# Optimization experiments

Hardware: AMD Instinct MI355X
Metric: run time of the kernel (lower is better)

## Reference

```python
import jax, jax.numpy as jnp
import numpy as np

K = 7
SIZE = (129, 129)


def _conv2d(x, w, b, pad):
    # x: NCHW, w: OIHW
    y = jax.lax.conv_general_dilated(
        x, w, window_strides=(1, 1), padding=[(pad, pad), (pad, pad)],
        dimension_numbers=("NCHW", "OIHW", "NCHW"))
    return y + b[None, :, None, None]


def _upsample_bilinear(x, size):
    # matches torch nn.Upsample(mode='bilinear', align_corners=False)
    b, c = x.shape[0], x.shape[1]
    return jax.image.resize(x, (b, c, size[0], size[1]), method="bilinear")


def _spatially_variant_conv(kernels, features, k):
    # kernels: [b,k,k,h,w], features: [b,c,h,w]
    # equivalent to unfold + einsum('bcklhw,bklhw->bchw') but without the
    # huge im2col intermediate: accumulate over the k*k shifted views.
    b, c, h, w = features.shape
    p = k // 2
    fp = jnp.pad(features, ((0, 0), (0, 0), (p, p), (p, p)))
    out = jnp.zeros_like(features)
    for i in range(k):
        for j in range(k):
            out = out + fp[:, :, i:i + h, j:j + w] * kernels[:, i, j][:, None]
    return out


def setup_inputs() -> dict:
    key = jax.random.key(0)
    ks = jax.random.split(key, 9)
    s = 0.05
    return {
        "current_frame_low_features": jax.random.normal(ks[0], (2, 128, 33, 33), jnp.float32),
        "key_frame_low_features": jax.random.normal(ks[1], (2, 128, 33, 33), jnp.float32),
        "key_frame_high_features": jax.random.normal(ks[2], (2, 256, 129, 129), jnp.float32),
        "w_reduce": jax.random.normal(ks[3], (256, 128, 3, 3), jnp.float32) * s,
        "b_reduce": jnp.zeros((256,), jnp.float32),
        "w_conv2": jax.random.normal(ks[4], (256, 512, 3, 3), jnp.float32) * s,
        "b_conv2": jnp.zeros((256,), jnp.float32),
        "w_conv3": jax.random.normal(ks[5], (K * K, 256, 1, 1), jnp.float32) * s,
        "b_conv3": jnp.zeros((K * K,), jnp.float32),
    }


def reference(current_frame_low_features, key_frame_low_features,
              key_frame_high_features, w_reduce, b_reduce,
              w_conv2, b_conv2, w_conv3, b_conv3):
    cur_up = _upsample_bilinear(current_frame_low_features, SIZE)
    key_up = _upsample_bilinear(key_frame_low_features, SIZE)

    # KernelWeightPredictor (shared conv_reduce weights for both frames)
    cur = jax.nn.relu(_conv2d(cur_up, w_reduce, b_reduce, 1))
    key = jax.nn.relu(_conv2d(key_up, w_reduce, b_reduce, 1))
    x = jax.nn.relu(_conv2d(jnp.concatenate((cur, key), axis=1), w_conv2, b_conv2, 1))
    x = jax.nn.relu(_conv2d(x, w_conv3, b_conv3, 0))
    x = jax.nn.softmax(x, axis=1)  # [b, k*k, H, W]
    b = x.shape[0]
    kernels = x.reshape(b, K, K, SIZE[0], SIZE[1])

    return _spatially_variant_conv(kernels, key_frame_high_features, K)
```

## Files before the change

kernel.cpp:

```cpp
#include <hip/hip_runtime.h>

typedef unsigned short u16;
typedef unsigned int   u32;
typedef __attribute__((ext_vector_type(8))) short s16x8;
typedef __attribute__((ext_vector_type(4))) float f32x4;
typedef __attribute__((ext_vector_type(4), aligned(4))) float f32x4u;
typedef __attribute__((ext_vector_type(4))) u32   u32x4;
typedef __attribute__((ext_vector_type(4))) u16   u16x4;

#define NPIX 16641
#define HP   131
#define FPH  135
#define FPW  136
#define FPC  18360


__device__ __forceinline__ u16 f2bf(float f) {
    u32 b = __builtin_bit_cast(u32, f);
    return (u16)((b + 0x7fffu + ((b >> 16) & 1u)) >> 16);
}
__device__ __forceinline__ float bf2f(u16 u) {
    return __builtin_bit_cast(float, ((u32)u) << 16);
}

__device__ __forceinline__ void async_cp16(const void* g, void* l) {
    __builtin_amdgcn_global_load_lds(
        (const __attribute__((address_space(1))) u32*)g,
        (__attribute__((address_space(3))) u32*)l, 16, 0, 0);
}

__global__ __launch_bounds__(256) void zero_border(u16* __restrict__ U,
                                                   u16* __restrict__ S1) {
    const int plane = blockIdx.y;
    const bool isU = plane < 4;
    const int C = isU ? 128 : 512;
    const int cpp = C / 8;
    int e = blockIdx.x * 256 + threadIdx.x;
    if (e >= 520 * cpp) return;
    int pix = e / cpp, ch = e - pix * cpp;
    int r, c;
    if (pix < 131)      { r = 0;   c = pix; }
    else if (pix < 262) { r = 130; c = pix - 131; }
    else { int j = pix - 262; r = 1 + (j >> 1); c = (j & 1) ? 130 : 0; }
    int img = isU ? plane : (plane - 4);
    u16* base = (isU ? U : S1) + ((long)(img * HP + r) * HP + c) * C + ch * 8;
    u32x4 z = {0u, 0u, 0u, 0u};
    *(u32x4*)base = z;
}

__global__ __launch_bounds__(256) void prep_weights(
        const float* __restrict__ wr, const float* __restrict__ w2,
        const float* __restrict__ w3,
        u16* __restrict__ Wt1, u16* __restrict__ Wt2, float* __restrict__ w3t) {
    int i = blockIdx.x * 256 + threadIdx.x;
    if (i < 294912) {
        int tap = i / 32768, r = i & 32767;
        int co = r >> 7, ci = r & 127;
        Wt1[i] = f2bf(wr[(co * 128 + ci) * 9 + tap]);
    } else if (i < 1474560) {
        int j = i - 294912;
        int tap = j / 131072, r = j & 131071;
        int co = r >> 9, ci = r & 511;
        Wt2[j] = f2bf(w2[(co * 512 + ci) * 9 + tap]);
    } else if (i < 1487104) {
        int j = i - 1474560;
        int c = j / 49, t = j - c * 49;
        w3t[j] = w3[t * 256 + c];
    }
}

__global__ __launch_bounds__(256) void upsample(
        const float* __restrict__ cur, const float* __restrict__ key,
        u16* __restrict__ U) {
    __shared__ float rows[2][128][33];
    const int y = blockIdx.x;
    const int img = blockIdx.y;
    const int frame = img >> 1, bb = img & 1;
    const float* src = (frame ? key : cur) + (long)bb * 128 * 1089;
    const float scale = 33.0f / 129.0f;
    float syf = (y + 0.5f) * scale - 0.5f;
    int sy0 = (int)floorf(syf);
    float wy = syf - (float)sy0;
    int sy0c = sy0 < 0 ? 0 : sy0;
    int sy1c = (sy0 + 1 > 32) ? 32 : sy0 + 1;
    for (int e = threadIdx.x; e < 2 * 128 * 33; e += 256) {
        int rr = e / 4224;
        int rem = e - rr * 4224;
        int c = rem / 33, sx = rem - c * 33;
        rows[rr][c][sx] = src[((long)c * 33 + (rr ? sy1c : sy0c)) * 33 + sx];
    }
    __syncthreads();
    u16* dst = U + ((long)(img * HP + (y + 1)) * HP + 1) * 128;
    for (int e = threadIdx.x; e < 129 * 128; e += 256) {
        int x = e >> 7, c = e & 127;
        float sxf = (x + 0.5f) * scale - 0.5f;
        int sx0 = (int)floorf(sxf);
        float wx = sxf - (float)sx0;
        int sx0c = sx0 < 0 ? 0 : sx0;
        int sx1c = (sx0 + 1 > 32) ? 32 : sx0 + 1;
        float v0 = rows[0][c][sx0c] * (1.f - wx) + rows[0][c][sx1c] * wx;
        float v1 = rows[1][c][sx0c] * (1.f - wx) + rows[1][c][sx1c] * wx;
        dst[(long)x * 128 + c] = f2bf(v0 * (1.f - wy) + v1 * wy);
    }
}

template<int CIN, int MODE, int NWORK, int SPLIT>
__global__ __launch_bounds__(256) void conv_mfma(
        const u16* __restrict__ In, const u16* __restrict__ Wt,
        const float* __restrict__ bias,
        u16* __restrict__ Out0, u16* __restrict__ Out1) {
    constexpr int KC  = CIN / 32;
    constexpr int NS  = 9 * KC;
    constexpr int NSH = NS / SPLIT;
    constexpr int PER = (NWORK + 7) / 8;
    __shared__ u16 As[3][128 * 32];
    __shared__ u16 Bs[3][128 * 32];

    const int id = blockIdx.x;
    const int work = (id & 7) * PER + (id >> 3);
    if (work >= NWORK) return;
    int w = work;
    const int m0 = (w & 1) * 128; w >>= 1;
    int half = 0;
    if (SPLIT == 2) { half = w & 1; w >>= 1; }
    const int xi  = w % 131;
    const int img = w / 131;
    const int p0  = xi * 128;

    const int t    = threadIdx.x;
    const int srow = t >> 2;
    const int scol = ((((t & 3) - (srow >> 1)) & 3) * 8);
    long ub[2];
    #pragma unroll
    for (int is = 0; is < 2; ++is) {
        int p = p0 + srow + is * 64; if (p > NPIX - 1) p = NPIX - 1;
        int y = p / 129, x = p - y * 129;
        ub[is] = ((long)(img * HP + y) * HP + x) * CIN + scol;
    }
    const long wb0 = (long)(m0 + srow) * CIN + scol;

    const int lane = t & 63;
    const int wave = t >> 6;
    const int wm = wave & 1, wn = wave >> 1;
    const int lm = lane & 15, lq = lane >> 4;
    const int koff = (((lq + (lm >> 1)) & 3) * 8);

    auto stage = [&](int s, int buf) {
        const int tap = s / KC;
        const int kc  = (s - tap * KC) * 32;
        const int ky = tap / 3, kx = tap - ky * 3;
        const long toff = (long)(ky * HP + kx) * CIN + kc;
        const u16* WtT = Wt + (long)tap * 256 * CIN + kc;
        char* Aw = (char*)&As[buf][0] + wave * 1024;
        char* Bw = (char*)&Bs[buf][0] + wave * 1024;
        async_cp16(WtT + wb0,             Aw);
        async_cp16(WtT + wb0 + 64L * CIN, Aw + 4096);
        async_cp16(In + ub[0] + toff,     Bw);
        async_cp16(In + ub[1] + toff,     Bw + 4096);
    };

    f32x4 acc[4][4];
    f32x4 zero = {0.f, 0.f, 0.f, 0.f};
    #pragma unroll
    for (int mt = 0; mt < 4; ++mt)
        #pragma unroll
        for (int nt = 0; nt < 4; ++nt) acc[mt][nt] = zero;

    const int s0 = half * NSH;
    stage(s0 + 0, 0);
    stage(s0 + 1, 1);
    #pragma unroll 2
    for (int i = 0; i < NSH; ++i) {
        const int buf = i % 3;
        if (i < NSH - 1) asm volatile("s_waitcnt vmcnt(4)" ::: "memory");
        else             asm volatile("s_waitcnt vmcnt(0)" ::: "memory");
        __builtin_amdgcn_s_barrier();
        asm volatile("" ::: "memory");
        if (i + 2 < NSH) stage(s0 + i + 2, (i + 2) % 3);
        s16x8 fa[4], fb[4];
        #pragma unroll
        for (int mt = 0; mt < 4; ++mt)
            fa[mt] = *(const s16x8*)&As[buf][(wm * 64 + mt * 16 + lm) * 32 + koff];
        #pragma unroll
        for (int nt = 0; nt < 4; ++nt)
            fb[nt] = *(const s16x8*)&Bs[buf][(wn * 64 + nt * 16 + lm) * 32 + koff];
        #pragma unroll
        for (int mt = 0; mt < 4; ++mt)
            #pragma unroll
            for (int nt = 0; nt < 4; ++nt)
                acc[mt][nt] = __builtin_amdgcn_mfma_f32_16x16x32_bf16(
                    fa[mt], fb[nt], acc[mt][nt], 0, 0, 0);
    }

    u16* OutBf = half ? Out1 : Out0;
    #pragma unroll
    for (int nt = 0; nt < 4; ++nt) {
        int p = p0 + wn * 64 + nt * 16 + lm;
        if (p > NPIX - 1) continue;
        long obase;
        if (MODE == 0) {
            int y = p / 129, x = p - y * 129;
            int bb = img & 1, frame = img >> 1;
            obase = ((long)(bb * HP + (y + 1)) * HP + (x + 1)) * 512 + frame * 256;
        } else {
            obase = ((long)img * NPIX + p) * 256;
        }
        #pragma unroll
        for (int mt = 0; mt < 4; ++mt) {
            int co = m0 + wm * 64 + mt * 16 + lq * 4;
            f32x4 bv = *(const f32x4*)(bias + co);
            if (MODE == 0) {
                float v0 = fmaxf(acc[mt][nt][0] + bv[0], 0.f);
                float v1 = fmaxf(acc[mt][nt][1] + bv[1], 0.f);
                float v2 = fmaxf(acc[mt][nt][2] + bv[2], 0.f);
                float v3 = fmaxf(acc[mt][nt][3] + bv[3], 0.f);
                u16x4 o = { f2bf(v0), f2bf(v1), f2bf(v2), f2bf(v3) };
                *(u16x4*)(OutBf + obase + co) = o;
            } else {
                float bs = half ? 0.f : 1.f;
                u16x4 o = { f2bf(acc[mt][nt][0] + bs * bv[0]),
                            f2bf(acc[mt][nt][1] + bs * bv[1]),
                            f2bf(acc[mt][nt][2] + bs * bv[2]),
                            f2bf(acc[mt][nt][3] + bs * bv[3]) };
                *(u16x4*)(OutBf + obase + co) = o;
            }
        }
    }
}

__global__ __launch_bounds__(256) void fpad(
        const float* __restrict__ F, float* __restrict__ Fp) {
    int id = blockIdx.x * 256 + threadIdx.x;
    if (id >= 2 * 256 * FPH * (FPW / 4)) return;
    int ck = id % (FPW / 4);
    int r  = id / (FPW / 4);
    int yy = r % FPH;
    int ch = r / FPH;
    int y = yy - 3;
    f32x4 v;
    const float* Fr = F + ((long)ch * 129 + y) * 129;
    #pragma unroll
    for (int j = 0; j < 4; ++j) {
        int x = ck * 4 + j - 3;
        bool in = ((unsigned)x < 129u) && ((unsigned)y < 129u);
        v[j] = in ? Fr[x] : 0.f;
    }
    *(f32x4*)(Fp + (long)ch * FPC + yy * FPW + ck * 4) = v;
}

__global__ __launch_bounds__(256) void conv3_softmax(
        const u16* __restrict__ Xa, const u16* __restrict__ Xb,
        const float* __restrict__ W3t, const float* __restrict__ b3,
        float* __restrict__ P) {
    __shared__ float red[3][64][50];
    const int t = threadIdx.x;
    const int pl = t & 63, sub = t >> 6;
    const int idx = blockIdx.x * 64 + pl;
    const bool valid = idx < 2 * NPIX;
    float l[49];
    #pragma unroll
    for (int k = 0; k < 49; ++k) l[k] = 0.f;
    if (valid) {
        const s16x8* xra = (const s16x8*)(Xa + (long)idx * 256 + sub * 64);
        const s16x8* xrb = (const s16x8*)(Xb + (long)idx * 256 + sub * 64);
        #pragma unroll 1
        for (int cb = 0; cb < 8; ++cb) {
            s16x8 av = xra[cb];
            s16x8 bv = xrb[cb];
            #pragma unroll
            for (int j = 0; j < 8; ++j) {
                float xc = fmaxf(bf2f((u16)av[j]) + bf2f((u16)bv[j]), 0.f);
                const float* wrow = W3t + (sub * 64 + cb * 8 + j) * 49;
                #pragma unroll
                for (int k = 0; k < 49; ++k) l[k] = fmaf(wrow[k], xc, l[k]);
            }
        }
    }
    if (sub) {
        #pragma unroll
        for (int k = 0; k < 49; ++k) red[sub - 1][pl][k] = l[k];
    }
    __syncthreads();
    if (!sub && valid) {
        float m = 0.f;
        #pragma unroll
        for (int k = 0; k < 49; ++k) {
            l[k] = fmaxf(l[k] + red[0][pl][k] + red[1][pl][k] + red[2][pl][k]
                         + b3[k], 0.f);
            m = fmaxf(m, l[k]);
        }
        float ssum = 0.f;
        #pragma unroll
        for (int k = 0; k < 49; ++k) { l[k] = __expf(l[k] - m); ssum += l[k]; }
        float inv = 1.f / ssum;
        int bb = idx / NPIX, pix = idx - bb * NPIX;
        float* Pp = P + ((long)bb * NPIX + pix) * 52;
        #pragma unroll
        for (int k = 0; k < 49; ++k) Pp[k] = l[k] * inv;
    }
}

__global__ __launch_bounds__(256) void svconv(
        const float* __restrict__ Fp, const float* __restrict__ P,
        float* __restrict__ Out) {
    const int id = blockIdx.x;
    const int work = (id & 7) * 1056 + (id >> 3);
    const int cg   = work & 63;
    const int tile = work >> 6;
    const int img  = tile / 66, ti = tile % 66;
    const int pix  = ti * 256 + threadIdx.x;
    if (pix >= NPIX) return;
    const int y = pix / 129, x = pix - y * 129;

    float w[52];
    const f32x4* Pp = (const f32x4*)(P + ((long)img * NPIX + pix) * 52);
    #pragma unroll
    for (int k = 0; k < 13; ++k) *(f32x4*)&w[k * 4] = Pp[k];

    const float* Fc0 = Fp + (long)(img * 256 + cg * 4) * FPC + (long)y * FPW + x;
    float acc[4];
    #pragma unroll
    for (int c4 = 0; c4 < 4; ++c4) {
        const float* Fc = Fc0 + c4 * FPC;
        float a = 0.f;
        #pragma unroll
        for (int ky = 0; ky < 7; ++ky) {
            const float* rp = Fc + ky * FPW;
            f32x4u v0 = *(const f32x4u*)rp;
            f32x4u v1 = *(const f32x4u*)(rp + 4);
            const float* wr = &w[ky * 7];
            a = fmaf(wr[0], v0[0], a);
            a = fmaf(wr[1], v0[1], a);
            a = fmaf(wr[2], v0[2], a);
            a = fmaf(wr[3], v0[3], a);
            a = fmaf(wr[4], v1[0], a);
            a = fmaf(wr[5], v1[1], a);
            a = fmaf(wr[6], v1[2], a);
        }
        acc[c4] = a;
    }
    float* Ob = Out + ((long)(img * 256 + cg * 4)) * NPIX + pix;
    Ob[0] = acc[0];
    Ob[(long)NPIX] = acc[1];
    Ob[2L * NPIX] = acc[2];
    Ob[3L * NPIX] = acc[3];
}

extern "C" void kernel_launch(void* const* d_in, const int* in_sizes, int n_in,
                              void* d_out, int out_size, void* d_ws, size_t ws_size,
                              hipStream_t stream) {
    const float* cur      = (const float*)d_in[0];
    const float* key      = (const float*)d_in[1];
    const float* Fhigh    = (const float*)d_in[2];
    const float* w_reduce = (const float*)d_in[3];
    const float* b_reduce = (const float*)d_in[4];
    const float* w_conv2  = (const float*)d_in[5];
    const float* b_conv2  = (const float*)d_in[6];
    const float* w_conv3  = (const float*)d_in[7];
    const float* b_conv3  = (const float*)d_in[8];

    if (ws_size < 89798656UL) return;

    char* ws = (char*)d_ws;
    u16*   U     = (u16*)(ws + 0);
    u16*   S1    = (u16*)(ws + 17572864);
    float* Fpad  = (float*)(ws + 0);
    float* P     = (float*)(ws + 37601280);
    u16*   Wt1   = (u16*)(ws + 52718592);
    u16*   Wt2   = (u16*)(ws + 53308416);
    u16*   out2a = (u16*)(ws + 55667712);
    u16*   out2b = (u16*)(ws + 72708096);
    float* w3t   = (float*)(ws + 89748480);

    zero_border<<<dim3(130, 6), 256, 0, stream>>>(U, S1);
    prep_weights<<<5809, 256, 0, stream>>>(w_reduce, w_conv2, w_conv3, Wt1, Wt2, w3t);
    upsample<<<dim3(129, 4), 256, 0, stream>>>(cur, key, U);
    conv_mfma<128, 0, 1048, 1><<<1048, 256, 0, stream>>>(U, Wt1, b_reduce, S1, S1);
    conv_mfma<512, 1, 1048, 2><<<1048, 256, 0, stream>>>(S1, Wt2, b_conv2, out2a, out2b);
    fpad<<<9180, 256, 0, stream>>>(Fhigh, Fpad);
    conv3_softmax<<<521, 256, 0, stream>>>(out2a, out2b, w3t, b_conv3, P);
    svconv<<<8448, 256, 0, stream>>>(Fpad, P, (float*)d_out);
}
```

Baseline: 487.0 us.

## Transpose padded features to channel-last and compute 2x2 pixel blocks in svconv

Replaces the NCHW padding kernel with a transpose-and-pad kernel that writes features as HWC (channel innermost) through shared memory. The spatially-variant conv is restructured so each wave handles a 2x2 pixel block across all 256 channels, with each lane holding 4 channels. This lets the blocked pixels share one pass over 8 input rows and 8 columns instead of reloading overlapping windows. Results are staged in LDS and transposed back to NCHW for coalesced stores. It adds an LDS transpose, more edge-case branching, and a larger 512-thread block.

```diff
diff --git a/kernel.cpp b/kernel.cpp
--- a/kernel.cpp
+++ b/kernel.cpp
@@ -10,9 +10,7 @@
 
 #define NPIX 16641
 #define HP   131
-#define FPH  135
-#define FPW  136
-#define FPC  18360
+#define FPY  135
 
 
 __device__ __forceinline__ u16 f2bf(float f) {
@@ -226,26 +224,6 @@
             }
         }
     }
-}
-
-__global__ __launch_bounds__(256) void fpad(
-        const float* __restrict__ F, float* __restrict__ Fp) {
-    int id = blockIdx.x * 256 + threadIdx.x;
-    if (id >= 2 * 256 * FPH * (FPW / 4)) return;
-    int ck = id % (FPW / 4);
-    int r  = id / (FPW / 4);
-    int yy = r % FPH;
-    int ch = r / FPH;
-    int y = yy - 3;
-    f32x4 v;
-    const float* Fr = F + ((long)ch * 129 + y) * 129;
-    #pragma unroll
-    for (int j = 0; j < 4; ++j) {
-        int x = ck * 4 + j - 3;
-        bool in = ((unsigned)x < 129u) && ((unsigned)y < 129u);
-        v[j] = in ? Fr[x] : 0.f;
-    }
-    *(f32x4*)(Fp + (long)ch * FPC + yy * FPW + ck * 4) = v;
 }
 
 __global__ __launch_bounds__(256) void conv3_softmax(
@@ -300,50 +278,126 @@
     }
 }
 
-__global__ __launch_bounds__(256) void svconv(
+__global__ __launch_bounds__(256) void tpad(
+        const float* __restrict__ F, float* __restrict__ Fp) {
+    __shared__ float T[64][133];
+    const int yyp = blockIdx.x;
+    const int img = blockIdx.y;
+    const int cb  = blockIdx.z;
+    const int t = threadIdx.x;
+    const int yo = yyp - 3;
+    float* dst = Fp + (((long)img * FPY + yyp) * FPY) * 256 + cb * 64;
+    if ((unsigned)yo > 128u) {
+        for (int e = t; e < FPY * 64; e += 256) {
+            int xx = e >> 6, c = e & 63;
+            dst[(long)xx * 256 + c] = 0.f;
+        }
+        return;
+    }
+    const float* src = F + ((long)(img * 256 + cb * 64)) * NPIX + yo * 129;
+    for (int e = t; e < 64 * 129; e += 256) {
+        int c = e / 129, x = e - c * 129;
+        T[c][x] = src[(long)c * NPIX + x];
+    }
+    __syncthreads();
+    for (int e = t; e < FPY * 64; e += 256) {
+        int xx = e >> 6, c = e & 63;
+        int xo = xx - 3;
+        dst[(long)xx * 256 + c] = ((unsigned)xo <= 128u) ? T[c][xo] : 0.f;
+    }
+}
+
+__global__ __launch_bounds__(512) void svconv(
         const float* __restrict__ Fp, const float* __restrict__ P,
         float* __restrict__ Out) {
-    const int id = blockIdx.x;
-    const int work = (id & 7) * 1056 + (id >> 3);
-    const int cg   = work & 63;
-    const int tile = work >> 6;
-    const int img  = tile / 66, ti = tile % 66;
-    const int pix  = ti * 256 + threadIdx.x;
-    if (pix >= NPIX) return;
-    const int y = pix / 129, x = pix - y * 129;
-
-    float w[52];
-    const f32x4* Pp = (const f32x4*)(P + ((long)img * NPIX + pix) * 52);
-    #pragma unroll
-    for (int k = 0; k < 13; ++k) *(f32x4*)&w[k * 4] = Pp[k];
-
-    const float* Fc0 = Fp + (long)(img * 256 + cg * 4) * FPC + (long)y * FPW + x;
-    float acc[4];
-    #pragma unroll
-    for (int c4 = 0; c4 < 4; ++c4) {
-        const float* Fc = Fc0 + c4 * FPC;
-        float a = 0.f;
-        #pragma unroll
-        for (int ky = 0; ky < 7; ++ky) {
-            const float* rp = Fc + ky * FPW;
-            f32x4u v0 = *(const f32x4u*)rp;
-            f32x4u v1 = *(const f32x4u*)(rp + 4);
-            const float* wr = &w[ky * 7];
-            a = fmaf(wr[0], v0[0], a);
-            a = fmaf(wr[1], v0[1], a);
-            a = fmaf(wr[2], v0[2], a);
-            a = fmaf(wr[3], v0[3], a);
-            a = fmaf(wr[4], v1[0], a);
-            a = fmaf(wr[5], v1[1], a);
-            a = fmaf(wr[6], v1[2], a);
-        }
-        acc[c4] = a;
-    }
-    float* Ob = Out + ((long)(img * 256 + cg * 4)) * NPIX + pix;
-    Ob[0] = acc[0];
-    Ob[(long)NPIX] = acc[1];
-    Ob[2L * NPIX] = acc[2];
-    Ob[3L * NPIX] = acc[3];
+    __shared__ float Ls[2][16][260];
+    const int id  = blockIdx.x;
+    const int img = id / 585;
+    const int rr  = id - img * 585;
+    const int yp  = rr / 9, xg = rr - yp * 9;
+    const int y   = 2 * yp;
+    const int tid = threadIdx.x;
+    const int lane = tid & 63, wv = tid >> 6;
+    const int x = xg * 16 + 2 * wv;
+    const bool has_y1 = (y < 128);
+    const bool active = (x <= 128);
+    const bool has_x1 = (x < 128);
+
+    if (active) {
+        const int px0 = y * 129 + x;
+        const float* Pw00 = P + ((long)img * NPIX + px0) * 52;
+        const float* Pw01 = Pw00 + 52;
+        const float* Pw10 = Pw00 + 129 * 52;
+        const float* Pw11 = Pw10 + 52;
+        const float* Fb = Fp + (((long)img * FPY + y) * FPY + x) * 256 + 4 * lane;
+
+        f32x4 z4 = {0.f, 0.f, 0.f, 0.f};
+        f32x4 acc00 = z4, acc01 = z4, acc10 = z4, acc11 = z4;
+        #pragma unroll
+        for (int r = 0; r < 8; ++r) {
+            if (r == 7 && !has_y1) break;
+            f32x4 a00 = z4, b00 = z4, a01 = z4, b01 = z4;
+            f32x4 a10 = z4, b10 = z4, a11 = z4, b11 = z4;
+            if (r < 7) {
+                a00 = *(const f32x4u*)(Pw00 + r * 7);
+                b00 = *(const f32x4u*)(Pw00 + r * 7 + 3);
+                if (has_x1) {
+                    a01 = *(const f32x4u*)(Pw01 + r * 7);
+                    b01 = *(const f32x4u*)(Pw01 + r * 7 + 3);
+                }
+            }
+            if (r >= 1 && has_y1) {
+                a10 = *(const f32x4u*)(Pw10 + (r - 1) * 7);
+                b10 = *(const f32x4u*)(Pw10 + (r - 1) * 7 + 3);
+                if (has_x1) {
+                    a11 = *(const f32x4u*)(Pw11 + (r - 1) * 7);
+                    b11 = *(const f32x4u*)(Pw11 + (r - 1) * 7 + 3);
+                }
+            }
+            const float* Fr = Fb + (long)r * FPY * 256;
+            f32x4 f[8];
+            #pragma unroll
+            for (int q = 0; q < 7; ++q) f[q] = *(const f32x4*)(Fr + q * 256);
+            if (has_x1) f[7] = *(const f32x4*)(Fr + 7 * 256);
+            else        f[7] = z4;
+            #pragma unroll
+            for (int q = 0; q < 8; ++q) {
+                if (q < 7) {
+                    float w0 = (q < 4) ? a00[q] : b00[q - 3];
+                    acc00 += w0 * f[q];
+                    float w2 = (q < 4) ? a10[q] : b10[q - 3];
+                    acc10 += w2 * f[q];
+                }
+                if (q >= 1) {
+                    const int k = q - 1;
+                    float w1 = (k < 4) ? a01[k] : b01[k - 3];
+                    acc01 += w1 * f[q];
+                    float w3 = (k < 4) ? a11[k] : b11[k - 3];
+                    acc11 += w3 * f[q];
+                }
+            }
+        }
+        const int xr = 2 * wv;
+        *(f32x4*)&Ls[0][xr    ][4 * lane] = acc00;
+        *(f32x4*)&Ls[0][xr + 1][4 * lane] = acc01;
+        *(f32x4*)&Ls[1][xr    ][4 * lane] = acc10;
+        *(f32x4*)&Ls[1][xr + 1][4 * lane] = acc11;
+    }
+    __syncthreads();
+
+    const int ch = tid & 255, dy = tid >> 8;
+    if (dy && !has_y1) return;
+    float* Ob = Out + ((long)(img * 256 + ch)) * NPIX + (y + dy) * 129 + xg * 16;
+    if (xg < 8) {
+        float o[16];
+        #pragma unroll
+        for (int xx = 0; xx < 16; ++xx) o[xx] = Ls[dy][xx][ch];
+        #pragma unroll
+        for (int k2 = 0; k2 < 4; ++k2)
+            *(f32x4u*)(Ob + 4 * k2) = *(f32x4*)&o[4 * k2];
+    } else {
+        Ob[0] = Ls[dy][0][ch];
+    }
 }
 
 extern "C" void kernel_launch(void* const* d_in, const int* in_sizes, int n_in,
@@ -364,7 +418,7 @@
     char* ws = (char*)d_ws;
     u16*   U     = (u16*)(ws + 0);
     u16*   S1    = (u16*)(ws + 17572864);
-    float* Fpad  = (float*)(ws + 0);
+    float* Fp    = (float*)(ws + 0);
     float* P     = (float*)(ws + 37601280);
     u16*   Wt1   = (u16*)(ws + 52718592);
     u16*   Wt2   = (u16*)(ws + 53308416);
@@ -377,7 +431,7 @@
     upsample<<<dim3(129, 4), 256, 0, stream>>>(cur, key, U);
     conv_mfma<128, 0, 1048, 1><<<1048, 256, 0, stream>>>(U, Wt1, b_reduce, S1, S1);
     conv_mfma<512, 1, 1048, 2><<<1048, 256, 0, stream>>>(S1, Wt2, b_conv2, out2a, out2b);
-    fpad<<<9180, 256, 0, stream>>>(Fhigh, Fpad);
+    tpad<<<dim3(FPY, 2, 4), 256, 0, stream>>>(Fhigh, Fp);
     conv3_softmax<<<521, 256, 0, stream>>>(out2a, out2b, w3t, b_conv3, P);
-    svconv<<<8448, 256, 0, stream>>>(Fpad, P, (float*)d_out);
-}
+    svconv<<<1170, 512, 0, stream>>>(Fp, P, (float*)d_out);
+}
```

Result: slower. 801.8 us (+64.6%).
